# Kernel tuning notes

Measured on AMD Instinct MI355X. Metric: run time of the kernel, lower is better.

Reference implementation:

```python
import jax, jax.numpy as jnp
import numpy as np
import math

N_HEAD = 16
N_EMBD = 1024
HEAD_D = N_EMBD // N_HEAD
BASE = 10000


def rope(Y):
    # Y: [b, h, t, d]; positions start at 1 as in the torch code
    d = Y.shape[-1]
    t = Y.shape[-2]
    theta = BASE ** (-2.0 * jnp.arange(d // 2, dtype=Y.dtype) / d)
    theta2 = jnp.concatenate([theta, theta], axis=0)          # [d]
    pos = jnp.arange(1, t + 1, dtype=Y.dtype)                 # [t]
    C = pos[:, None] * theta2[None, :]                        # [t, d]
    cos, sin = jnp.cos(C), jnp.sin(C)
    Y2 = jnp.concatenate([-Y[..., d // 2:], Y[..., : d // 2]], axis=-1)
    return Y * cos + Y2 * sin


def setup_inputs() -> dict:
    key = jax.random.key(0)
    ks = jax.random.split(key, 9)
    s = 0.02
    x = jax.random.normal(ks[0], (4, 2048, N_EMBD), dtype=jnp.float32)
    Wq = jax.random.normal(ks[1], (N_EMBD, N_EMBD), dtype=jnp.float32) * s
    bq = jnp.zeros((N_EMBD,), dtype=jnp.float32)
    Wk = jax.random.normal(ks[2], (N_EMBD, N_EMBD), dtype=jnp.float32) * s
    bk = jnp.zeros((N_EMBD,), dtype=jnp.float32)
    Wv = jax.random.normal(ks[3], (N_EMBD, N_EMBD), dtype=jnp.float32) * s
    bv = jnp.zeros((N_EMBD,), dtype=jnp.float32)
    Wo = jax.random.normal(ks[4], (N_EMBD, N_EMBD), dtype=jnp.float32) * s
    bo = jnp.zeros((N_EMBD,), dtype=jnp.float32)
    return {"x": x, "Wq": Wq, "bq": bq, "Wk": Wk, "bk": bk,
            "Wv": Wv, "bv": bv, "Wo": Wo, "bo": bo}


def reference(x, Wq, bq, Wk, bk, Wv, bv, Wo, bo):
    b, t, _ = x.shape
    def split_heads(y):
        return y.reshape(b, t, N_HEAD, HEAD_D).transpose(0, 2, 1, 3)  # b h t d
    q = split_heads(x @ Wq.T + bq)
    k = split_heads(x @ Wk.T + bk)
    v = split_heads(x @ Wv.T + bv)
    q, k = rope(q), rope(k)
    scale = math.sqrt(HEAD_D)
    att = jnp.einsum('bhqd,bhkd->bhqk', q, k) / scale
    mask = jnp.tril(jnp.ones((t, t), dtype=bool))
    att = jnp.where(mask, att, -jnp.inf)
    att = jax.nn.softmax(att, axis=-1)
    y = jnp.einsum('bhqk,bhkd->bhqd', att, v)
    y = y.transpose(0, 2, 1, 3).reshape(b, t, N_EMBD)
    return y @ Wo.T + bo
```

## Files before the change

### kernel.cpp

```cpp
#include <hip/hip_runtime.h>
#include <hip/hip_bf16.h>
#include <cstdint>

typedef __attribute__((ext_vector_type(8))) short short8;
typedef __attribute__((ext_vector_type(4))) short short4v;
typedef __attribute__((ext_vector_type(4))) float f32x4;
typedef __attribute__((ext_vector_type(16))) float f32x16;
typedef __attribute__((ext_vector_type(4))) unsigned int u32x4;
typedef unsigned short ushort_t;
typedef unsigned int uint32;

#define DEVI static __device__ __forceinline__

DEVI ushort_t f2bf(float f){
  uint32 u = __builtin_bit_cast(uint32, f);
  u += 0x7FFFu + ((u >> 16) & 1u);
  return (ushort_t)(u >> 16);
}
DEVI float bf2f(ushort_t s){
  uint32 u = ((uint32)s) << 16;
  return __builtin_bit_cast(float, u);
}
DEVI uint32 cvtpk_bf16(float lo, float hi){
  uint32 r;
  asm("v_cvt_pk_bf16_f32 %0, %1, %2" : "=v"(r) : "v"(lo), "v"(hi));
  return r;
}
DEVI void plswap(uint32& a, uint32& b){
  asm("v_permlane32_swap_b32 %0, %1" : "+v"(a), "+v"(b));
}

typedef __attribute__((address_space(1))) const uint32 g_u32;
typedef __attribute__((address_space(3))) uint32 l_u32;
#define GL_LDS16(gp, lp) __builtin_amdgcn_global_load_lds((g_u32*)(gp), (l_u32*)(lp), 16, 0, 0)

__global__ __launch_bounds__(256) void convert_all(
    const float* __restrict__ x, const float* __restrict__ wq, const float* __restrict__ wk,
    const float* __restrict__ wv, const float* __restrict__ wo,
    ushort_t* __restrict__ xb, ushort_t* __restrict__ wqkv, ushort_t* __restrict__ wob){
  int bid = blockIdx.x;
  const float* src; ushort_t* dst; long base;
  if (bid < 4096){ src = x; dst = xb; base = (long)bid * 2048; }
  else {
    int r = bid - 4096; int sel = r >> 9; int o = r & 511;
    src = sel==0?wq: sel==1?wk: sel==2?wv: wo;
    dst = (sel<3) ? (wqkv + (long)sel * 1048576) : wob;
    base = (long)o * 2048;
  }
  long i = base + (long)threadIdx.x * 8;
  const float* p = src + i;
  float4 a = *(const float4*)p;
  float4 b = *(const float4*)(p + 4);
  short8 v;
  v[0]=(short)f2bf(a.x); v[1]=(short)f2bf(a.y); v[2]=(short)f2bf(a.z); v[3]=(short)f2bf(a.w);
  v[4]=(short)f2bf(b.x); v[5]=(short)f2bf(b.y); v[6]=(short)f2bf(b.z); v[7]=(short)f2bf(b.w);
  *(short8*)(dst + i) = v;
}

__global__ __launch_bounds__(256) void rope_table(float2* __restrict__ tab){
  const int idx = blockIdx.x * 256 + threadIdx.x;
  const int tok = idx >> 5, j = idx & 31;
  const float theta = exp2f(-(float)j * 0.4152410118609203f);
  const float ang = (float)(tok + 1) * theta;
  float s, c;
  sincosf(ang, &s, &c);
  tab[idx] = make_float2(c, s);
}

__global__ __launch_bounds__(512, 2) void gemm256_qkv(
    const ushort_t* __restrict__ A, const ushort_t* __restrict__ Bw,
    const float* __restrict__ bq, const float* __restrict__ bk, const float* __restrict__ bv,
    const float2* __restrict__ tab,
    ushort_t* __restrict__ Qb, ushort_t* __restrict__ Kb, ushort_t* __restrict__ Vt){
  __shared__ __align__(16) ushort_t S[49152];
  const int tid = threadIdx.x;
  const int w = tid >> 6, l = tid & 63, lr = l & 15, lg = l >> 4;
  const int wm = w >> 2, wn = w & 3;
  const int bid = (blockIdx.x & 7) * 48 + (blockIdx.x >> 3);
  const int bm = bid / 12, bn = bid % 12;
  const int m0 = bm << 8, n0 = bn << 8;
  const int srow = tid >> 2;
  const int swzc = (tid & 3) ^ (srow & 3) ^ ((srow >> 2) & 3);
  const ushort_t* aS = A  + (long)(m0 + srow) * 1024 + swzc * 8;
  const ushort_t* bS = Bw + (long)(n0 + srow) * 1024 + swzc * 8;
  const int sw = (lr & 3) ^ ((lr >> 2) & 3);
  const int aOff = ((wm << 7) + lr) * 32 + ((lg ^ sw) << 3);
  const int bOff = 8192 + ((wn << 6) + lr) * 32 + ((lg ^ sw) << 3);
  f32x4 acc[8][4] = {};

#define STG(matOff, src, t, bf_) do{ \
    GL_LDS16((src) + (long)(t)*32,          &S[(bf_)*16384 + (matOff) + tid*8]); \
    GL_LDS16((src) + (long)(t)*32 + 131072, &S[(bf_)*16384 + (matOff) + 4096 + tid*8]); }while(0)

  STG(0, aS, 0, 0); STG(8192, bS, 0, 0);
  STG(0, aS, 1, 1); STG(8192, bS, 1, 1);
  asm volatile("s_waitcnt vmcnt(4)" ::: "memory");
  __builtin_amdgcn_s_barrier();

  int buf = 0;
  for (int t = 0; t < 32; ++t){
    const int nbuf = (buf == 0) ? 2 : buf - 1;
    const ushort_t* Sb = &S[buf * 16384];
    short8 af[8], bf0[2];
#pragma unroll
    for (int mi = 0; mi < 8; ++mi) af[mi] = *(const short8*)&Sb[aOff + mi * 512];
    bf0[0] = *(const short8*)&Sb[bOff];
    bf0[1] = *(const short8*)&Sb[bOff + 512];
    if (t < 30) STG(0, aS, t + 2, nbuf);
    __builtin_amdgcn_s_barrier();
    __builtin_amdgcn_s_setprio(1);
#pragma unroll
    for (int mi = 0; mi < 8; ++mi){
      acc[mi][0] = __builtin_amdgcn_mfma_f32_16x16x32_bf16(af[mi], bf0[0], acc[mi][0], 0, 0, 0);
      acc[mi][1] = __builtin_amdgcn_mfma_f32_16x16x32_bf16(af[mi], bf0[1], acc[mi][1], 0, 0, 0);
    }
    __builtin_amdgcn_s_setprio(0);
    __builtin_amdgcn_s_barrier();
    short8 bf1[2];
    bf1[0] = *(const short8*)&Sb[bOff + 1024];
    bf1[1] = *(const short8*)&Sb[bOff + 1536];
    if (t < 30) STG(8192, bS, t + 2, nbuf);
    __builtin_amdgcn_s_barrier();
    __builtin_amdgcn_s_setprio(1);
#pragma unroll
    for (int mi = 0; mi < 8; ++mi){
      acc[mi][2] = __builtin_amdgcn_mfma_f32_16x16x32_bf16(af[mi], bf1[0], acc[mi][2], 0, 0, 0);
      acc[mi][3] = __builtin_amdgcn_mfma_f32_16x16x32_bf16(af[mi], bf1[1], acc[mi][3], 0, 0, 0);
    }
    __builtin_amdgcn_s_setprio(0);
    if (t < 30) asm volatile("s_waitcnt vmcnt(4)" ::: "memory");
    else        asm volatile("s_waitcnt vmcnt(0)" ::: "memory");
    __builtin_amdgcn_s_barrier();
    buf = (buf == 2) ? 0 : buf + 1;
  }
#undef STG

  const int colX = n0 + (wn << 6);
  const int sel = colX >> 10;
  const int h = (colX >> 6) & 15;
  const int cB = (colX & 1023) + lr;
  if (sel < 2){
    ushort_t* dst = sel ? Kb : Qb;
    const float* bp = sel ? bk : bq;
    const float bvs[4] = {bp[cB], bp[cB+16], bp[cB+32], bp[cB+48]};
#pragma unroll
    for (int mi = 0; mi < 8; ++mi){
      const int row0 = m0 + (wm << 7) + mi*16 + lg*4;
#pragma unroll
      for (int i = 0; i < 4; ++i){
        const int r = row0 + i;
        const int b = r >> 11, tok = r & 2047;
#pragma unroll
        for (int nc = 0; nc < 2; ++nc){
          const int j = nc*16 + lr;
          const float2 cs = tab[tok*32 + j];
          const float v0 = acc[mi][nc][i]   + bvs[nc];
          const float v1 = acc[mi][nc+2][i] + bvs[nc+2];
          const long base = (((long)((b<<4) + h) * 2048 + tok) << 6) + j;
          dst[base]      = f2bf(v0 * cs.x - v1 * cs.y);
          dst[base + 32] = f2bf(v1 * cs.x + v0 * cs.y);
        }
      }
    }
  } else {
    const float bvs[4] = {bv[cB], bv[cB+16], bv[cB+32], bv[cB+48]};
#pragma unroll
    for (int mi = 0; mi < 8; ++mi){
      const int row0 = m0 + (wm << 7) + mi*16 + lg*4;
#pragma unroll
      for (int nc = 0; nc < 4; ++nc){
        const int d = nc*16 + lr;
#pragma unroll
        for (int i = 0; i < 4; ++i){
          const int r = row0 + i;
          const int b = r >> 11, tok = r & 2047;
          Vt[((long)((b<<4) + h) * 64 + d) * 2048 + tok] = f2bf(acc[mi][nc][i] + bvs[nc]);
        }
      }
    }
  }
}

__global__ __launch_bounds__(256) void gemm_out(
    const ushort_t* __restrict__ A, const ushort_t* __restrict__ Bw,
    const float* __restrict__ bias, float* __restrict__ Cout){
  __shared__ ushort_t As[4096];
  __shared__ ushort_t Bs[4096];
  const int tid = threadIdx.x, l = tid & 63, w = tid >> 6;
  const int lr = l & 15, lg = l >> 4;
  const int bid = (blockIdx.x & 7) * 64 + (blockIdx.x >> 3);
  const int bm = bid >> 3, bn = bid & 7;
  const int m0 = bm << 7, n0 = bn << 7;
  const int wm = (w >> 1) << 6, wn = (w & 1) << 6;
  f32x4 acc[4][4] = {};
  const ushort_t* aS = A + (long)(m0 + (tid >> 2)) * 1024 + (tid & 3) * 8;
  const ushort_t* bS = Bw + (long)(n0 + (tid >> 2)) * 1024 + (tid & 3) * 8;
  const long skip = (long)64 * 1024;
  for (int kt = 0; kt < 32; ++kt){
    GL_LDS16(aS,        &As[w * 512]);
    GL_LDS16(aS + skip, &As[2048 + w * 512]);
    GL_LDS16(bS,        &Bs[w * 512]);
    GL_LDS16(bS + skip, &Bs[2048 + w * 512]);
    aS += 32; bS += 32;
    __syncthreads();
    short8 af[4], bfr[4];
#pragma unroll
    for (int mi = 0; mi < 4; ++mi) af[mi]  = *(const short8*)&As[(wm + mi*16 + lr)*32 + lg*8];
#pragma unroll
    for (int ni = 0; ni < 4; ++ni) bfr[ni] = *(const short8*)&Bs[(wn + ni*16 + lr)*32 + lg*8];
#pragma unroll
    for (int mi = 0; mi < 4; ++mi)
#pragma unroll
      for (int ni = 0; ni < 4; ++ni)
        acc[mi][ni] = __builtin_amdgcn_mfma_f32_16x16x32_bf16(af[mi], bfr[ni], acc[mi][ni], 0, 0, 0);
    __syncthreads();
  }
  const int colBase = n0 + wn + lr;
#pragma unroll
  for (int mi = 0; mi < 4; ++mi){
    const int row0 = m0 + wm + mi*16 + lg*4;
#pragma unroll
    for (int ni = 0; ni < 4; ++ni){
      const int col = colBase + ni*16;
      const float bvv = bias[col];
#pragma unroll
      for (int i = 0; i < 4; ++i)
        Cout[(long)(row0 + i) * 1024 + col] = acc[mi][ni][i] + bvv;
    }
  }
}

__global__ __launch_bounds__(512, 4) void attn(
    const ushort_t* __restrict__ Qb, const ushort_t* __restrict__ Kb,
    const ushort_t* __restrict__ Vt, ushort_t* __restrict__ yb){
  __shared__ __align__(16) ushort_t Ks[2][2048];
  __shared__ __align__(16) ushort_t Vs[2][2048];
  const int tid = threadIdx.x;
  const int w = tid >> 6, l = tid & 63;
  const int lq = l & 31;
  const int hi = l >> 5;
  const int xcd = blockIdx.x & 7;
  const int idx = blockIdx.x >> 3;
  const int hi5 = idx >> 5;
  const int bh  = (xcd << 3) + ((idx >> 3) & 3) + hi5 * 4;
  const int qj  = hi5 ? (idx & 7) : 7 - (idx & 7);
  const int qc = (qj << 3) + w;
  const int q0 = qc << 5;
  const int ktmax = (qj << 3) + 7;
  const ushort_t* Qh = Qb + (long)bh * 2048 * 64;
  const ushort_t* Kh = Kb + (long)bh * 2048 * 64;
  const ushort_t* Vth = Vt + (long)bh * 64 * 2048;
  const int h8 = hi * 8;

  const ushort_t* qp = &Qh[(long)(q0 + lq) * 64 + h8];
  short8 qf0 = *(const short8*)(qp);
  short8 qf1 = *(const short8*)(qp + 16);
  short8 qf2 = *(const short8*)(qp + 32);
  short8 qf3 = *(const short8*)(qp + 48);

  const int stg_is_v = (w >= 4);
  long stg_src_off; int stg_dst_off;
  if (!stg_is_v){
    const int row = (w << 3) + (l >> 3);
    const int cl  = (l & 7) ^ (row & 7);
    stg_src_off = ((long)row << 6) + (cl << 3);
    stg_dst_off = (w << 9) + (l << 3);
  } else {
    const int row = ((w - 4) << 3) + (l >> 3);
    const int cl  = (l & 7) ^ (row & 7);
    const int dd  = row + ((cl & 4) << 3);
    stg_src_off = ((long)dd << 11) + ((cl & 3) << 3);
    stg_dst_off = ((w - 4) << 9) + (l << 3);
  }

  f32x16 o0 = {}, o1 = {};
  float lsum = 0.f;
  const float cl2 = 0.1803368801111204f;

  if (!stg_is_v) GL_LDS16(Kh + stg_src_off,  &Ks[0][stg_dst_off]);
  else           GL_LDS16(Vth + stg_src_off, &Vs[0][stg_dst_off]);
  __syncthreads();

  int cur = 0;
  for (int kt = 0; kt <= ktmax; ++kt){
    if (kt < ktmax){
      const int k0n = (kt + 1) << 5;
      if (!stg_is_v) GL_LDS16(Kh + ((long)k0n << 6) + stg_src_off, &Ks[cur ^ 1][stg_dst_off]);
      else           GL_LDS16(Vth + k0n + stg_src_off,             &Vs[cur ^ 1][stg_dst_off]);
    }
    if (kt <= qc){
      const int swk = lq & 7;
      const ushort_t* kr = &Ks[cur][lq << 6];
      short8 kf0 = *(const short8*)&kr[((hi    ) ^ swk) << 3];
      short8 kf1 = *(const short8*)&kr[((2 + hi) ^ swk) << 3];
      short8 kf2 = *(const short8*)&kr[((4 + hi) ^ swk) << 3];
      short8 kf3 = *(const short8*)&kr[((6 + hi) ^ swk) << 3];
      const ushort_t* vr = &Vs[cur][lq << 6];
      short8 vf00 = *(const short8*)&vr[((hi    ) ^ swk) << 3];
      short8 vf01 = *(const short8*)&vr[((2 + hi) ^ swk) << 3];
      short8 vf10 = *(const short8*)&vr[((4 + hi) ^ swk) << 3];
      short8 vf11 = *(const short8*)&vr[((6 + hi) ^ swk) << 3];
      f32x16 s = {};
      s = __builtin_amdgcn_mfma_f32_32x32x16_bf16(kf0, qf0, s, 0, 0, 0);
      s = __builtin_amdgcn_mfma_f32_32x32x16_bf16(kf1, qf1, s, 0, 0, 0);
      s = __builtin_amdgcn_mfma_f32_32x32x16_bf16(kf2, qf2, s, 0, 0, 0);
      s = __builtin_amdgcn_mfma_f32_32x32x16_bf16(kf3, qf3, s, 0, 0, 0);
      if (kt == qc){
#pragma unroll
        for (int r = 0; r < 16; ++r){
          const int rk = (r & 3) + 8 * (r >> 2) + 4 * hi;
          if (rk > lq) s[r] = -1e30f;
        }
      }
#pragma unroll
      for (int r = 0; r < 16; ++r) s[r] = __builtin_amdgcn_exp2f(__builtin_fmaf(s[r], cl2, -2.0f));
      {
        float t0 = (s[0] + s[1]) + (s[2] + s[3]);
        float t1 = (s[4] + s[5]) + (s[6] + s[7]);
        float t2 = (s[8] + s[9]) + (s[10] + s[11]);
        float t3 = (s[12] + s[13]) + (s[14] + s[15]);
        lsum += (t0 + t1) + (t2 + t3);
      }
      uint32 a0 = cvtpk_bf16(s[0], s[1]),  b0 = cvtpk_bf16(s[4], s[5]);
      uint32 a1 = cvtpk_bf16(s[2], s[3]),  b1 = cvtpk_bf16(s[6], s[7]);
      uint32 a2 = cvtpk_bf16(s[8], s[9]),  b2 = cvtpk_bf16(s[12], s[13]);
      uint32 a3 = cvtpk_bf16(s[10], s[11]),b3 = cvtpk_bf16(s[14], s[15]);
      plswap(a0, b0);
      plswap(a1, b1);
      plswap(a2, b2);
      plswap(a3, b3);
      u32x4 pc0 = {a0, a1, b0, b1};
      u32x4 pc1 = {a2, a3, b2, b3};
      short8 pb0 = __builtin_bit_cast(short8, pc0);
      short8 pb1 = __builtin_bit_cast(short8, pc1);
      o0 = __builtin_amdgcn_mfma_f32_32x32x16_bf16(vf00, pb0, o0, 0, 0, 0);
      o0 = __builtin_amdgcn_mfma_f32_32x32x16_bf16(vf01, pb1, o0, 0, 0, 0);
      o1 = __builtin_amdgcn_mfma_f32_32x32x16_bf16(vf10, pb0, o1, 0, 0, 0);
      o1 = __builtin_amdgcn_mfma_f32_32x32x16_bf16(vf11, pb1, o1, 0, 0, 0);
    }
    __syncthreads();
    cur ^= 1;
  }
  lsum += __shfl_xor(lsum, 32);
  const float inv = 1.0f / lsum;
  const int b = bh >> 4, h = bh & 15;
  const int tok = q0 + lq;
  ushort_t* yrow = yb + (long)(b * 2048 + tok) * 1024 + h * 64;
#pragma unroll
  for (int g = 0; g < 4; ++g){
    short4v p0, p1;
#pragma unroll
    for (int j = 0; j < 4; ++j){
      p0[j] = (short)f2bf(o0[4*g + j] * inv);
      p1[j] = (short)f2bf(o1[4*g + j] * inv);
    }
    *(short4v*)&yrow[8*g + 4*hi]      = p0;
    *(short4v*)&yrow[32 + 8*g + 4*hi] = p1;
  }
}

extern "C" void kernel_launch(void* const* d_in, const int* in_sizes, int n_in,
                              void* d_out, int out_size, void* d_ws, size_t ws_size,
                              hipStream_t stream){
  const float* x  = (const float*)d_in[0];
  const float* Wq = (const float*)d_in[1];
  const float* bq = (const float*)d_in[2];
  const float* Wk = (const float*)d_in[3];
  const float* bk = (const float*)d_in[4];
  const float* Wv = (const float*)d_in[5];
  const float* bv = (const float*)d_in[6];
  const float* Wo = (const float*)d_in[7];
  const float* bo = (const float*)d_in[8];
  char* ws = (char*)d_ws;
  ushort_t* xb   = (ushort_t*)(ws);
  ushort_t* wqkv = (ushort_t*)(ws + 16777216);
  ushort_t* wob  = (ushort_t*)(ws + 23068672);
  float2*   tab  = (float2*)  (ws + 25165824);
  ushort_t* Qb   = (ushort_t*)(ws + 25690112);
  ushort_t* Kb   = (ushort_t*)(ws + 42467328);
  ushort_t* Vt   = (ushort_t*)(ws + 59244544);
  ushort_t* yb   = xb;

  convert_all<<<6144, 256, 0, stream>>>(x, Wq, Wk, Wv, Wo, xb, wqkv, wob);
  rope_table<<<256, 256, 0, stream>>>(tab);
  gemm256_qkv<<<384, 512, 0, stream>>>(xb, wqkv, bq, bk, bv, tab, Qb, Kb, Vt);
  attn<<<512, 512, 0, stream>>>(Qb, Kb, Vt, yb);
  gemm_out<<<512, 256, 0, stream>>>(yb, wob, bo, (float*)d_out);
}
```

Before: 171.3 us.

## Restructure QKV GEMM into double-buffered 64-wide K stages with new LDS swizzle

The fused QKV projection GEMM moves from a triple-buffered pipeline with 32-wide K tiles to a double-buffered pipeline with 64-wide K tiles. Each 64-wide tile is split into two 32-wide halves, and loads for the next tile are interleaved with the MFMA phases. The loop trip count halves, which cuts the number of waits and barriers per unit of work, and the LDS swizzle pattern changes to reduce bank conflicts. LDS use grows to 128 KB per block, which limits residency and leaves only one tile of prefetch lookahead.

New measurement: 161.9 us. -5.4%, faster.

```diff
diff --git a/kernel.cpp b/kernel.cpp
--- a/kernel.cpp
+++ b/kernel.cpp
@@ -33,6 +33,8 @@
 typedef __attribute__((address_space(1))) const uint32 g_u32;
 typedef __attribute__((address_space(3))) uint32 l_u32;
 #define GL_LDS16(gp, lp) __builtin_amdgcn_global_load_lds((g_u32*)(gp), (l_u32*)(lp), 16, 0, 0)
+
+#define MFMA16(a, b, c) __builtin_amdgcn_mfma_f32_16x16x32_bf16(a, b, c, 0, 0, 0)
 
 __global__ __launch_bounds__(256) void convert_all(
     const float* __restrict__ x, const float* __restrict__ wq, const float* __restrict__ wk,
@@ -72,66 +74,93 @@
     const float* __restrict__ bq, const float* __restrict__ bk, const float* __restrict__ bv,
     const float2* __restrict__ tab,
     ushort_t* __restrict__ Qb, ushort_t* __restrict__ Kb, ushort_t* __restrict__ Vt){
-  __shared__ __align__(16) ushort_t S[49152];
+  __shared__ __align__(16) ushort_t S[65536];
   const int tid = threadIdx.x;
   const int w = tid >> 6, l = tid & 63, lr = l & 15, lg = l >> 4;
   const int wm = w >> 2, wn = w & 3;
   const int bid = (blockIdx.x & 7) * 48 + (blockIdx.x >> 3);
   const int bm = bid / 12, bn = bid % 12;
   const int m0 = bm << 8, n0 = bn << 8;
-  const int srow = tid >> 2;
-  const int swzc = (tid & 3) ^ (srow & 3) ^ ((srow >> 2) & 3);
-  const ushort_t* aS = A  + (long)(m0 + srow) * 1024 + swzc * 8;
-  const ushort_t* bS = Bw + (long)(n0 + srow) * 1024 + swzc * 8;
-  const int sw = (lr & 3) ^ ((lr >> 2) & 3);
-  const int aOff = ((wm << 7) + lr) * 32 + ((lg ^ sw) << 3);
-  const int bOff = 8192 + ((wn << 6) + lr) * 32 + ((lg ^ sw) << 3);
+  const int rbase = tid >> 2;
+  const int swzk = (tid & 3) ^ ((tid >> 3) & 3);
+  const ushort_t* aS = A  + (long)(m0 + rbase) * 1024 + swzk * 8;
+  const ushort_t* bS = Bw + (long)(n0 + rbase) * 1024 + swzk * 8;
+  const int slot = (lg ^ ((lr >> 1) & 3)) << 3;
+  const int arow = wm * 128 + lr;
+  const int brow = wn * 64 + lr;
   f32x4 acc[8][4] = {};
 
-#define STG(matOff, src, t, bf_) do{ \
-    GL_LDS16((src) + (long)(t)*32,          &S[(bf_)*16384 + (matOff) + tid*8]); \
-    GL_LDS16((src) + (long)(t)*32 + 131072, &S[(bf_)*16384 + (matOff) + 4096 + tid*8]); }while(0)
-
-  STG(0, aS, 0, 0); STG(8192, bS, 0, 0);
-  STG(0, aS, 1, 1); STG(8192, bS, 1, 1);
+#define STG(isB, kk, t, bf_) do{ \
+    const ushort_t* _s = ((isB) ? bS : aS) + (long)(t)*64 + (kk)*32; \
+    ushort_t* _d = &S[(bf_)*32768 + (isB)*16384 + (kk)*8192 + tid*8]; \
+    GL_LDS16(_s,          _d); \
+    GL_LDS16(_s + 131072, _d + 4096); }while(0)
+
+  STG(0,0,0,0); STG(1,0,0,0); STG(0,1,0,0); STG(1,1,0,0);
   asm volatile("s_waitcnt vmcnt(4)" ::: "memory");
   __builtin_amdgcn_s_barrier();
 
-  int buf = 0;
-  for (int t = 0; t < 32; ++t){
-    const int nbuf = (buf == 0) ? 2 : buf - 1;
-    const ushort_t* Sb = &S[buf * 16384];
-    short8 af[8], bf0[2];
-#pragma unroll
-    for (int mi = 0; mi < 8; ++mi) af[mi] = *(const short8*)&Sb[aOff + mi * 512];
-    bf0[0] = *(const short8*)&Sb[bOff];
-    bf0[1] = *(const short8*)&Sb[bOff + 512];
-    if (t < 30) STG(0, aS, t + 2, nbuf);
+  short8 af[8], bf0, bf1;
+  for (int t = 0; t < 16; ++t){
+    const int buf = t & 1, nbuf = buf ^ 1;
+    const bool last = (t == 15);
+    const ushort_t* SA = &S[buf * 32768];
+    const ushort_t* SB = &S[buf * 32768 + 16384];
+#pragma unroll
+    for (int f = 0; f < 8; ++f) af[f] = *(const short8*)&SA[(arow + f*16)*32 + slot];
+    bf0 = *(const short8*)&SB[(brow     )*32 + slot];
+    bf1 = *(const short8*)&SB[(brow + 16)*32 + slot];
+    if (!last) STG(0,0,t+1,nbuf);
     __builtin_amdgcn_s_barrier();
     __builtin_amdgcn_s_setprio(1);
 #pragma unroll
-    for (int mi = 0; mi < 8; ++mi){
-      acc[mi][0] = __builtin_amdgcn_mfma_f32_16x16x32_bf16(af[mi], bf0[0], acc[mi][0], 0, 0, 0);
-      acc[mi][1] = __builtin_amdgcn_mfma_f32_16x16x32_bf16(af[mi], bf0[1], acc[mi][1], 0, 0, 0);
+    for (int f = 0; f < 8; ++f){
+      acc[f][0] = MFMA16(af[f], bf0, acc[f][0]);
+      acc[f][1] = MFMA16(af[f], bf1, acc[f][1]);
     }
     __builtin_amdgcn_s_setprio(0);
     __builtin_amdgcn_s_barrier();
-    short8 bf1[2];
-    bf1[0] = *(const short8*)&Sb[bOff + 1024];
-    bf1[1] = *(const short8*)&Sb[bOff + 1536];
-    if (t < 30) STG(8192, bS, t + 2, nbuf);
+    bf0 = *(const short8*)&SB[(brow + 32)*32 + slot];
+    bf1 = *(const short8*)&SB[(brow + 48)*32 + slot];
+    if (!last) STG(1,0,t+1,nbuf);
     __builtin_amdgcn_s_barrier();
     __builtin_amdgcn_s_setprio(1);
 #pragma unroll
-    for (int mi = 0; mi < 8; ++mi){
-      acc[mi][2] = __builtin_amdgcn_mfma_f32_16x16x32_bf16(af[mi], bf1[0], acc[mi][2], 0, 0, 0);
-      acc[mi][3] = __builtin_amdgcn_mfma_f32_16x16x32_bf16(af[mi], bf1[1], acc[mi][3], 0, 0, 0);
+    for (int f = 0; f < 8; ++f){
+      acc[f][2] = MFMA16(af[f], bf0, acc[f][2]);
+      acc[f][3] = MFMA16(af[f], bf1, acc[f][3]);
     }
     __builtin_amdgcn_s_setprio(0);
-    if (t < 30) asm volatile("s_waitcnt vmcnt(4)" ::: "memory");
-    else        asm volatile("s_waitcnt vmcnt(0)" ::: "memory");
-    __builtin_amdgcn_s_barrier();
-    buf = (buf == 2) ? 0 : buf + 1;
+    if (!last) asm volatile("s_waitcnt vmcnt(4)" ::: "memory");
+    else       asm volatile("s_waitcnt vmcnt(0)" ::: "memory");
+    __builtin_amdgcn_s_barrier();
+#pragma unroll
+    for (int f = 0; f < 8; ++f) af[f] = *(const short8*)&SA[8192 + (arow + f*16)*32 + slot];
+    bf0 = *(const short8*)&SB[8192 + (brow     )*32 + slot];
+    bf1 = *(const short8*)&SB[8192 + (brow + 16)*32 + slot];
+    if (!last) STG(0,1,t+1,nbuf);
+    __builtin_amdgcn_s_barrier();
+    __builtin_amdgcn_s_setprio(1);
+#pragma unroll
+    for (int f = 0; f < 8; ++f){
+      acc[f][0] = MFMA16(af[f], bf0, acc[f][0]);
+      acc[f][1] = MFMA16(af[f], bf1, acc[f][1]);
+    }
+    __builtin_amdgcn_s_setprio(0);
+    __builtin_amdgcn_s_barrier();
+    bf0 = *(const short8*)&SB[8192 + (brow + 32)*32 + slot];
+    bf1 = *(const short8*)&SB[8192 + (brow + 48)*32 + slot];
+    if (!last) STG(1,1,t+1,nbuf);
+    __builtin_amdgcn_s_barrier();
+    __builtin_amdgcn_s_setprio(1);
+#pragma unroll
+    for (int f = 0; f < 8; ++f){
+      acc[f][2] = MFMA16(af[f], bf0, acc[f][2]);
+      acc[f][3] = MFMA16(af[f], bf1, acc[f][3]);
+    }
+    __builtin_amdgcn_s_setprio(0);
+    if (!last) asm volatile("s_waitcnt vmcnt(4)" ::: "memory");
+    __builtin_amdgcn_s_barrier();
   }
 #undef STG
 
@@ -212,7 +241,7 @@
     for (int mi = 0; mi < 4; ++mi)
 #pragma unroll
       for (int ni = 0; ni < 4; ++ni)
-        acc[mi][ni] = __builtin_amdgcn_mfma_f32_16x16x32_bf16(af[mi], bfr[ni], acc[mi][ni], 0, 0, 0);
+        acc[mi][ni] = MFMA16(af[mi], bfr[ni], acc[mi][ni]);
     __syncthreads();
   }
   const int colBase = n0 + wn + lr;
```

## Retile QKV GEMM to 256x128 blocks with 64-wide K steps

Applied to the files above, without the earlier changes.

The QKV projection GEMM drops from 256x256 tiles to 256x128 tiles, launching 768 blocks instead of 384. Each iteration now stages a 64-wide K slice as two 32-wide halves across a 3-stage LDS ring, and uses a new XOR swizzle and a 2x4 wave layout with 64x64 per-wave sub-tiles. The aim is better load balance across compute units and fewer barrier-synchronised iterations. In exchange, each tile reuses less data, LDS use per block grows, and per-wave accumulators shrink.

Measured after the change: 165.3 us. 3.5% less time.

```diff
diff --git a/kernel.cpp b/kernel.cpp
--- a/kernel.cpp
+++ b/kernel.cpp
@@ -33,6 +33,8 @@
 typedef __attribute__((address_space(1))) const uint32 g_u32;
 typedef __attribute__((address_space(3))) uint32 l_u32;
 #define GL_LDS16(gp, lp) __builtin_amdgcn_global_load_lds((g_u32*)(gp), (l_u32*)(lp), 16, 0, 0)
+
+#define MFMA16(a, b, c) __builtin_amdgcn_mfma_f32_16x16x32_bf16(a, b, c, 0, 0, 0)
 
 __global__ __launch_bounds__(256) void convert_all(
     const float* __restrict__ x, const float* __restrict__ wq, const float* __restrict__ wk,
@@ -67,73 +69,81 @@
   tab[idx] = make_float2(c, s);
 }
 
-__global__ __launch_bounds__(512, 2) void gemm256_qkv(
+__global__ __launch_bounds__(512, 2) void gemm_qkv(
     const ushort_t* __restrict__ A, const ushort_t* __restrict__ Bw,
     const float* __restrict__ bq, const float* __restrict__ bk, const float* __restrict__ bv,
     const float2* __restrict__ tab,
     ushort_t* __restrict__ Qb, ushort_t* __restrict__ Kb, ushort_t* __restrict__ Vt){
-  __shared__ __align__(16) ushort_t S[49152];
+  __shared__ __align__(16) ushort_t S[73728];
   const int tid = threadIdx.x;
   const int w = tid >> 6, l = tid & 63, lr = l & 15, lg = l >> 4;
-  const int wm = w >> 2, wn = w & 3;
-  const int bid = (blockIdx.x & 7) * 48 + (blockIdx.x >> 3);
-  const int bm = bid / 12, bn = bid % 12;
-  const int m0 = bm << 8, n0 = bn << 8;
-  const int srow = tid >> 2;
-  const int swzc = (tid & 3) ^ (srow & 3) ^ ((srow >> 2) & 3);
-  const ushort_t* aS = A  + (long)(m0 + srow) * 1024 + swzc * 8;
-  const ushort_t* bS = Bw + (long)(n0 + srow) * 1024 + swzc * 8;
-  const int sw = (lr & 3) ^ ((lr >> 2) & 3);
-  const int aOff = ((wm << 7) + lr) * 32 + ((lg ^ sw) << 3);
-  const int bOff = 8192 + ((wn << 6) + lr) * 32 + ((lg ^ sw) << 3);
-  f32x4 acc[8][4] = {};
-
-#define STG(matOff, src, t, bf_) do{ \
-    GL_LDS16((src) + (long)(t)*32,          &S[(bf_)*16384 + (matOff) + tid*8]); \
-    GL_LDS16((src) + (long)(t)*32 + 131072, &S[(bf_)*16384 + (matOff) + 4096 + tid*8]); }while(0)
-
-  STG(0, aS, 0, 0); STG(8192, bS, 0, 0);
-  STG(0, aS, 1, 1); STG(8192, bS, 1, 1);
-  asm volatile("s_waitcnt vmcnt(4)" ::: "memory");
+  const int wm = w >> 1, wn = w & 1;
+  const int bid = (blockIdx.x & 7) * 96 + (blockIdx.x >> 3);
+  const int bm = bid / 24, bn = bid % 24;
+  const int m0 = bm << 8, n0 = bn << 7;
+  const int rbase = tid >> 2;
+  const int swzk = (tid & 3) ^ ((tid >> 3) & 3);
+  const ushort_t* aS = A  + (long)(m0 + rbase) * 1024 + swzk * 8;
+  const ushort_t* bS = Bw + (long)(n0 + rbase) * 1024 + swzk * 8;
+  const int slot = (lg ^ ((lr >> 1) & 3)) << 3;
+  const int arow = wm * 64 + lr;
+  const int brow = wn * 64 + lr;
+  f32x4 acc[4][4] = {};
+
+#define STGA(kk, t, bf_) do{ \
+    const ushort_t* _s = aS + (long)(t)*64 + (kk)*32; \
+    ushort_t* _d = &S[(bf_)*24576 + (kk)*8192 + tid*8]; \
+    GL_LDS16(_s,          _d); \
+    GL_LDS16(_s + 131072, _d + 4096); }while(0)
+#define STGB(kk, t, bf_) do{ \
+    GL_LDS16(bS + (long)(t)*64 + (kk)*32, \
+             &S[(bf_)*24576 + 16384 + (kk)*4096 + tid*8]); }while(0)
+
+  STGA(0,0,0); STGB(0,0,0); STGA(1,0,0); STGB(1,0,0);
+  STGA(0,1,1); STGB(0,1,1); STGA(1,1,1); STGB(1,1,1);
+  asm volatile("s_waitcnt vmcnt(6)" ::: "memory");
   __builtin_amdgcn_s_barrier();
 
   int buf = 0;
-  for (int t = 0; t < 32; ++t){
-    const int nbuf = (buf == 0) ? 2 : buf - 1;
-    const ushort_t* Sb = &S[buf * 16384];
-    short8 af[8], bf0[2];
-#pragma unroll
-    for (int mi = 0; mi < 8; ++mi) af[mi] = *(const short8*)&Sb[aOff + mi * 512];
-    bf0[0] = *(const short8*)&Sb[bOff];
-    bf0[1] = *(const short8*)&Sb[bOff + 512];
-    if (t < 30) STG(0, aS, t + 2, nbuf);
+  for (int t = 0; t < 16; ++t){
+    const int nstg = (buf >= 1) ? buf - 1 : 2;
+    const ushort_t* SA = &S[buf * 24576];
+    const ushort_t* SB = &S[buf * 24576 + 16384];
+    short8 af[4], bfv[4];
+#pragma unroll
+    for (int mi = 0; mi < 4; ++mi) af[mi]  = *(const short8*)&SA[(arow + mi*16)*32 + slot];
+#pragma unroll
+    for (int nc = 0; nc < 4; ++nc) bfv[nc] = *(const short8*)&SB[(brow + nc*16)*32 + slot];
+    if (t < 14){ STGA(0, t+2, nstg); STGB(0, t+2, nstg); }
     __builtin_amdgcn_s_barrier();
     __builtin_amdgcn_s_setprio(1);
 #pragma unroll
-    for (int mi = 0; mi < 8; ++mi){
-      acc[mi][0] = __builtin_amdgcn_mfma_f32_16x16x32_bf16(af[mi], bf0[0], acc[mi][0], 0, 0, 0);
-      acc[mi][1] = __builtin_amdgcn_mfma_f32_16x16x32_bf16(af[mi], bf0[1], acc[mi][1], 0, 0, 0);
-    }
+    for (int mi = 0; mi < 4; ++mi)
+#pragma unroll
+      for (int nc = 0; nc < 4; ++nc)
+        acc[mi][nc] = MFMA16(af[mi], bfv[nc], acc[mi][nc]);
     __builtin_amdgcn_s_setprio(0);
     __builtin_amdgcn_s_barrier();
-    short8 bf1[2];
-    bf1[0] = *(const short8*)&Sb[bOff + 1024];
-    bf1[1] = *(const short8*)&Sb[bOff + 1536];
-    if (t < 30) STG(8192, bS, t + 2, nbuf);
+#pragma unroll
+    for (int mi = 0; mi < 4; ++mi) af[mi]  = *(const short8*)&SA[8192 + (arow + mi*16)*32 + slot];
+#pragma unroll
+    for (int nc = 0; nc < 4; ++nc) bfv[nc] = *(const short8*)&SB[4096 + (brow + nc*16)*32 + slot];
+    if (t < 14){ STGA(1, t+2, nstg); STGB(1, t+2, nstg); }
     __builtin_amdgcn_s_barrier();
     __builtin_amdgcn_s_setprio(1);
 #pragma unroll
-    for (int mi = 0; mi < 8; ++mi){
-      acc[mi][2] = __builtin_amdgcn_mfma_f32_16x16x32_bf16(af[mi], bf1[0], acc[mi][2], 0, 0, 0);
-      acc[mi][3] = __builtin_amdgcn_mfma_f32_16x16x32_bf16(af[mi], bf1[1], acc[mi][3], 0, 0, 0);
-    }
+    for (int mi = 0; mi < 4; ++mi)
+#pragma unroll
+      for (int nc = 0; nc < 4; ++nc)
+        acc[mi][nc] = MFMA16(af[mi], bfv[nc], acc[mi][nc]);
     __builtin_amdgcn_s_setprio(0);
-    if (t < 30) asm volatile("s_waitcnt vmcnt(4)" ::: "memory");
-    else        asm volatile("s_waitcnt vmcnt(0)" ::: "memory");
+    if (t < 14)       asm volatile("s_waitcnt vmcnt(6)" ::: "memory");
+    else if (t == 14) asm volatile("s_waitcnt vmcnt(0)" ::: "memory");
     __builtin_amdgcn_s_barrier();
-    buf = (buf == 2) ? 0 : buf + 1;
-  }
-#undef STG
+    buf = (buf >= 2) ? 0 : buf + 1;
+  }
+#undef STGA
+#undef STGB
 
   const int colX = n0 + (wn << 6);
   const int sel = colX >> 10;
@@ -144,8 +154,8 @@
     const float* bp = sel ? bk : bq;
     const float bvs[4] = {bp[cB], bp[cB+16], bp[cB+32], bp[cB+48]};
 #pragma unroll
-    for (int mi = 0; mi < 8; ++mi){
-      const int row0 = m0 + (wm << 7) + mi*16 + lg*4;
+    for (int mi = 0; mi < 4; ++mi){
+      const int row0 = m0 + (wm << 6) + mi*16 + lg*4;
 #pragma unroll
       for (int i = 0; i < 4; ++i){
         const int r = row0 + i;
@@ -165,8 +175,8 @@
   } else {
     const float bvs[4] = {bv[cB], bv[cB+16], bv[cB+32], bv[cB+48]};
 #pragma unroll
-    for (int mi = 0; mi < 8; ++mi){
-      const int row0 = m0 + (wm << 7) + mi*16 + lg*4;
+    for (int mi = 0; mi < 4; ++mi){
+      const int row0 = m0 + (wm << 6) + mi*16 + lg*4;
 #pragma unroll
       for (int nc = 0; nc < 4; ++nc){
         const int d = nc*16 + lr;
@@ -212,7 +222,7 @@
     for (int mi = 0; mi < 4; ++mi)
 #pragma unroll
       for (int ni = 0; ni < 4; ++ni)
-        acc[mi][ni] = __builtin_amdgcn_mfma_f32_16x16x32_bf16(af[mi], bfr[ni], acc[mi][ni], 0, 0, 0);
+        acc[mi][ni] = MFMA16(af[mi], bfr[ni], acc[mi][ni]);
     __syncthreads();
   }
   const int colBase = n0 + wn + lr;
@@ -383,7 +393,7 @@
 
   convert_all<<<6144, 256, 0, stream>>>(x, Wq, Wk, Wv, Wo, xb, wqkv, wob);
   rope_table<<<256, 256, 0, stream>>>(tab);
-  gemm256_qkv<<<384, 512, 0, stream>>>(xb, wqkv, bq, bk, bv, tab, Qb, Kb, Vt);
+  gemm_qkv<<<768, 512, 0, stream>>>(xb, wqkv, bq, bk, bv, tab, Qb, Kb, Vt);
   attn<<<512, 512, 0, stream>>>(Qb, Kb, Vt, yb);
   gemm_out<<<512, 256, 0, stream>>>(yb, wob, bo, (float*)d_out);
 }
```
